# Kernel optimization log

Hardware: AMD Instinct MI355X
Metric: run time of the kernel (lower is better)

The kernel has to match this reference:

```python
import jax, jax.numpy as jnp
import numpy as np
from jax import lax

B, C, H, W = 16, 128, 64, 64
S = 16  # d_state


def setup_inputs() -> dict:
    key = jax.random.key(0)
    ks = jax.random.split(key, 12)
    d = {
        'x': jax.random.normal(ks[0], (B, C, H, W), jnp.float32),
        'conv_w': jax.random.normal(ks[1], (C, C, 3, 3), jnp.float32) * (1.0 / np.sqrt(C * 9)),
        'conv_b': jax.random.normal(ks[2], (C,), jnp.float32) * 0.01,
        'dt_w': jax.random.normal(ks[3], (C, C), jnp.float32) * (1.0 / np.sqrt(C)),
        'dt_b': jax.random.normal(ks[4], (C,), jnp.float32) * 0.01,
        'A': jax.random.normal(ks[5], (C, S), jnp.float32),
        'D': jax.random.normal(ks[6], (C,), jnp.float32),
        'g1_w': jax.random.normal(ks[7], (C, C), jnp.float32) * (1.0 / np.sqrt(C)),
        'g1_b': jax.random.normal(ks[8], (C,), jnp.float32) * 0.01,
        'g2_w': jax.random.normal(ks[9], (C, C), jnp.float32) * (1.0 / np.sqrt(C)),
        'g2_b': jax.random.normal(ks[10], (C,), jnp.float32) * 0.01,
    }
    return d


def _forward(x, conv_w, conv_b, dt_w, dt_b, A, D, g1_w, g1_b, g2_w, g2_b):
    identity = x
    # 3x3 conv, padding=1 (SAME)
    x = lax.conv_general_dilated(x, conv_w, (1, 1), 'SAME',
                                 dimension_numbers=('NCHW', 'OIHW', 'NCHW'))
    x = x + conv_b[None, :, None, None]
    # spectral gate: global avg pool -> 1x1 conv -> relu -> 1x1 conv -> sigmoid
    pooled = jnp.mean(x, axis=(2, 3))                       # [B, C]
    g = jax.nn.relu(jnp.einsum('bc,oc->bo', pooled, g1_w) + g1_b)
    g = jax.nn.sigmoid(jnp.einsum('bc,oc->bo', g, g2_w) + g2_b)
    x = x * g[:, :, None, None]
    # ssm scan over H*W tokens
    x_seq = x.transpose(0, 2, 3, 1).reshape(x.shape[0], H * W, C)  # [B, L, C]
    dt = jax.nn.sigmoid(jnp.einsum('blc,oc->blo', x_seq, dt_w) + dt_b)
    An = -jnp.exp(A)   # [C, S]
    Dp = jnp.exp(D)    # [C]

    def step(h, inp):
        xt, dtt = inp  # each [B, C]
        h = h * jnp.exp(An[None] * dtt[:, :, None]) + xt[:, :, None]  # [B, C, S]
        y = jnp.sum(h * An[None], axis=-1) + Dp * xt                   # [B, C]
        return h, y

    h0 = jnp.zeros((x.shape[0], C, S), x.dtype)
    xs = (x_seq.transpose(1, 0, 2), dt.transpose(1, 0, 2))  # [L, B, C]
    _, ys = lax.scan(step, h0, xs)                           # ys: [L, B, C]
    y = ys.transpose(1, 0, 2).reshape(x.shape[0], H, W, C).transpose(0, 3, 1, 2)
    return y + identity


def reference(x, conv_w, conv_b, dt_w, dt_b, A, D, g1_w, g1_b, g2_w, g2_b):
    return _forward(x, conv_w, conv_b, dt_w, dt_b, A, D, g1_w, g1_b, g2_w, g2_b)
```

## Files before the change

### kernel.cpp

```cpp
#include <hip/hip_runtime.h>
#include <hip/hip_bf16.h>
#include <stdint.h>

#define BB 16
#define CC 128
#define HH 64
#define WW 64
#define LL 4096
#define SS 16
#define NCH 64
#define CT 64

typedef __attribute__((ext_vector_type(2))) float f32x2;
typedef __attribute__((ext_vector_type(4))) float f32x4;
typedef __attribute__((ext_vector_type(8))) short short8;
typedef __attribute__((ext_vector_type(4))) unsigned int u32x4;

#define AS1 __attribute__((address_space(1)))
#define AS3 __attribute__((address_space(3)))

__device__ __forceinline__ float bf2f(unsigned short u) {
    union { unsigned int i; float f; } v;
    v.i = ((unsigned int)u) << 16;
    return v.f;
}
__device__ __forceinline__ float asf(unsigned int u) {
    union { unsigned int i; float f; } v;
    v.i = u;
    return v.f;
}
__device__ __forceinline__ unsigned short f2bf(float f) {
    union { float f; unsigned int i; } v;
    v.f = f;
    unsigned int x = v.i;
    return (unsigned short)((x + 0x7fffu + ((x >> 16) & 1u)) >> 16);
}
__device__ __forceinline__ float fexp2(float x) { return __builtin_amdgcn_exp2f(x); }

__global__ __launch_bounds__(256) void k0(const float* __restrict__ x, unsigned short* __restrict__ xT,
                                          const float* __restrict__ conv_w, const float* __restrict__ dt_w,
                                          const float* __restrict__ A, const float* __restrict__ Dv,
                                          const float* __restrict__ g1w, const float* __restrict__ g2w,
                                          short* __restrict__ wf, short* __restrict__ wdtf,
                                          float* __restrict__ An, float* __restrict__ An2, float* __restrict__ Dp,
                                          float* __restrict__ pooled, float* __restrict__ g1wT, float* __restrict__ g2wT) {
    __shared__ float lt[64][65];
    int bid = blockIdx.x;
    int tid = threadIdx.x;
    if (bid < 2048) {
        int b = bid >> 7, rem = bid & 127;
        int tt = rem >> 1, ct = rem & 1;
        int t0 = tt * 64, c0 = ct * 64;
        int colr = tid & 63, rowb = tid >> 6;
#pragma unroll
        for (int r = 0; r < 16; ++r) {
            int row = rowb + r * 4;
            lt[row][colr] = x[(size_t)(b * CC + c0 + row) * LL + t0 + colr];
        }
        __syncthreads();
#pragma unroll
        for (int r = 0; r < 16; ++r) {
            int trow = rowb + r * 4;
            xT[((size_t)b * LL + t0 + trow) * CC + c0 + colr] = f2bf(lt[colr][trow]);
        }
        return;
    }
    int idx = (bid - 2048) * 256 + tid;
    if (idx < 18432) {
        int lane = idx & 63, fr = idx >> 6;
        int nfg = fr & 7, ks = (fr >> 3) & 3, tp = fr >> 5;
        int dy = tp / 3, dx = tp % 3;
        int cout = nfg * 16 + (lane & 15);
        int cin0 = ks * 32 + (lane >> 4) * 8;
        short8 v;
#pragma unroll
        for (int j = 0; j < 8; ++j)
            v[j] = (short)f2bf(conv_w[((cout * CC + cin0 + j) * 3 + dy) * 3 + dx]);
        *(short8*)(wf + (size_t)idx * 8) = v;
    } else if (idx < 20480) {
        int i2 = idx - 18432;
        int lane = i2 & 63, fr = i2 >> 6;
        int nfg = fr & 7, ks = fr >> 3;
        int o = nfg * 16 + (lane & 15);
        int c0 = ks * 32 + (lane >> 4) * 8;
        short8 v;
#pragma unroll
        for (int j = 0; j < 8; ++j) v[j] = (short)f2bf(dt_w[o * CC + c0 + j]);
        *(short8*)(wdtf + (size_t)i2 * 8) = v;
    } else if (idx < 22528) {
        int i3 = idx - 20480;
        float a = -expf(A[i3]);
        An[i3] = a;
        An2[i3] = a * 1.4426950408889634f;
    } else if (idx < 22656) {
        int c = idx - 22528;
        Dp[c] = expf(Dv[c]);
    } else if (idx < 24704) {
        pooled[idx - 22656] = 0.f;
    } else if (idx < 41088) {
        int i = idx - 24704;
        int c = i >> 7, o = i & 127;
        g1wT[i] = g1w[o * 128 + c];
    } else if (idx < 57472) {
        int i = idx - 41088;
        int c = i >> 7, o = i & 127;
        g2wT[i] = g2w[o * 128 + c];
    }
}

__global__ __launch_bounds__(256) void k1(const unsigned short* __restrict__ xT,
                                          const short* __restrict__ wf,
                                          const float* __restrict__ conv_b,
                                          unsigned short* __restrict__ convT,
                                          float* __restrict__ pooled) {
    __shared__ __align__(16) unsigned short slab[3 * 66 * 128];
    int bid = blockIdx.x;
    int b = bid >> 6, h = bid & 63;
    int tid = threadIdx.x;
    int wave = tid >> 6, lane = tid & 63;

    if (tid < 96) {
        int dy = tid >> 5, r = (tid >> 4) & 1, j = tid & 15;
        u32x4 z = {0, 0, 0, 0};
        *(u32x4*)((char*)slab + dy * 16896 + (r ? 16640 : 0) + j * 16) = z;
    }
#pragma unroll
    for (int dy = 0; dy < 3; ++dy) {
        int hs = h + dy - 1;
        char* slabdy = (char*)slab + dy * 16896;
        if (hs >= 0 && hs < HH) {
            const char* src = (const char*)xT + (size_t)(b * LL + hs * 64) * 256;
#pragma unroll
            for (int i = 0; i < 4; ++i) {
                unsigned int Xbase = 256u + (unsigned)i * 4096u + (unsigned)wave * 1024u;
                unsigned int X = Xbase + (unsigned)lane * 16u;
                unsigned int tok = X >> 8;
                unsigned int srcoff = ((X & ~255u) - 256u) | ((X & 255u) ^ ((tok & 7u) << 4));
                __builtin_amdgcn_global_load_lds((const AS1 unsigned int*)(src + srcoff),
                                                 (AS3 unsigned int*)(slabdy + Xbase), 16, 0, 0);
            }
        } else {
            u32x4 z = {0, 0, 0, 0};
#pragma unroll
            for (int i = 0; i < 4; ++i)
                *(u32x4*)(slabdy + 256 + tid * 64 + i * 16) = z;
        }
    }
    __syncthreads();

    int lm = lane & 15, lg = lane >> 4;
    f32x4 acc[4][2];
#pragma unroll
    for (int m = 0; m < 4; ++m)
#pragma unroll
        for (int n = 0; n < 2; ++n) acc[m][n] = (f32x4){0.f, 0.f, 0.f, 0.f};

#pragma unroll
    for (int tp = 0; tp < 9; ++tp) {
        int dy = tp / 3, dx = tp % 3;
        const char* slabdy = (const char*)slab + dy * 16896;
#pragma unroll
        for (int ks = 0; ks < 4; ++ks) {
            short8 bf0 = *(const short8*)(wf + ((size_t)(((tp * 4 + ks) * 8) + wave * 2 + 0) * 64 + lane) * 8);
            short8 bf1 = *(const short8*)(wf + ((size_t)(((tp * 4 + ks) * 8) + wave * 2 + 1) * 64 + lane) * 8);
#pragma unroll
            for (int mf = 0; mf < 4; ++mf) {
                int tok = mf * 16 + lm + dx;
                unsigned int off = (unsigned)((tok * 256 + ks * 64 + lg * 16) ^ ((tok & 7) << 4));
                short8 af = *(const short8*)(slabdy + off);
                acc[mf][0] = __builtin_amdgcn_mfma_f32_16x16x32_bf16(af, bf0, acc[mf][0], 0, 0, 0);
                acc[mf][1] = __builtin_amdgcn_mfma_f32_16x16x32_bf16(af, bf1, acc[mf][1], 0, 0, 0);
            }
        }
    }

    int n0w = wave * 32;
    size_t tokbase = (size_t)(b * LL + h * 64);
    float psum[2] = {0.f, 0.f};
#pragma unroll
    for (int nf = 0; nf < 2; ++nf) {
        int n = n0w + nf * 16 + lm;
        float bias = conv_b[n];
#pragma unroll
        for (int mf = 0; mf < 4; ++mf)
#pragma unroll
            for (int r = 0; r < 4; ++r) {
                int w = mf * 16 + lg * 4 + r;
                float v = acc[mf][nf][r] + bias;
                convT[(tokbase + w) * CC + n] = f2bf(v);
                psum[nf] += v;
            }
    }
#pragma unroll
    for (int nf = 0; nf < 2; ++nf) {
        float s = psum[nf];
        s += __shfl_xor(s, 16);
        s += __shfl_xor(s, 32);
        if (lane < 16) atomicAdd(&pooled[b * CC + n0w + nf * 16 + lane], s);
    }
}

__global__ __launch_bounds__(256) void k3(const unsigned short* __restrict__ convT,
                                          const short* __restrict__ wdtf,
                                          const float* __restrict__ pooled,
                                          const float* __restrict__ g1wT, const float* __restrict__ g1b,
                                          const float* __restrict__ g2wT, const float* __restrict__ g2b,
                                          float* __restrict__ gate,
                                          const float* __restrict__ dt_b,
                                          const float* __restrict__ An2,
                                          unsigned short* __restrict__ dtT,
                                          unsigned int* __restrict__ xdt,
                                          float* __restrict__ hend, float* __restrict__ decay,
                                          int packed) {
    __shared__ __align__(16) unsigned short albuf[128 * 128];
    __shared__ __align__(16) unsigned short dtl[128 * 136];
    __shared__ float gl[128];
    float* meanr = (float*)dtl;
    float* garr  = ((float*)dtl) + 128;
    int bid = blockIdx.x;
    int b = bid >> 5, tile = bid & 31, t0 = tile * 128;
    int tid = threadIdx.x;
    int wave = tid >> 6, lane = tid & 63;

    if (tid < 128) meanr[tid] = pooled[b * CC + tid] * (1.f / 4096.f);
    __syncthreads();
    if (tid < 128) {
        float acc = g1b[tid];
        for (int c = 0; c < 128; ++c) acc += meanr[c] * g1wT[c * 128 + tid];
        garr[tid] = fmaxf(acc, 0.f);
    }
    __syncthreads();
    if (tid < 128) {
        float acc2 = g2b[tid];
        for (int c = 0; c < 128; ++c) acc2 += garr[c] * g2wT[c * 128 + tid];
        float gv = __builtin_amdgcn_rcpf(1.f + fexp2(-1.4426950408889634f * acc2));
        gl[tid] = gv;
        if (tile == 0) gate[b * CC + tid] = gv;
    }
    __syncthreads();

    const char* srcb = (const char*)convT + (size_t)(b * LL + t0) * 256;
#pragma unroll
    for (int i = 0; i < 8; ++i) {
        unsigned int byteoff = (unsigned)((i * 256 + tid) * 16);
        unsigned int tok = byteoff >> 8;
        unsigned int inner = byteoff & 255u;
        int c8 = (int)(inner >> 1);
        short8 v = *(const short8*)(srcb + (size_t)tok * 256 + inner);
#pragma unroll
        for (int j = 0; j < 8; ++j) {
            float f = bf2f((unsigned short)v[j]) * gl[c8 + j];
            v[j] = (short)f2bf(f);
        }
        *(short8*)((char*)albuf + (byteoff ^ ((tok & 7u) << 4))) = v;
    }
    __syncthreads();

    int lm = lane & 15, lg = lane >> 4;
    f32x4 acc[8][2];
#pragma unroll
    for (int m = 0; m < 8; ++m)
#pragma unroll
        for (int n = 0; n < 2; ++n) acc[m][n] = (f32x4){0.f, 0.f, 0.f, 0.f};
#pragma unroll
    for (int ks = 0; ks < 4; ++ks) {
        short8 bf0 = *(const short8*)(wdtf + ((size_t)((ks * 8) + wave * 2 + 0) * 64 + lane) * 8);
        short8 bf1 = *(const short8*)(wdtf + ((size_t)((ks * 8) + wave * 2 + 1) * 64 + lane) * 8);
#pragma unroll
        for (int mf = 0; mf < 8; ++mf) {
            int tok = mf * 16 + lm;
            unsigned int off = (unsigned)((tok * 256 + ks * 64 + lg * 16) ^ ((tok & 7) << 4));
            short8 af = *(const short8*)((const char*)albuf + off);
            acc[mf][0] = __builtin_amdgcn_mfma_f32_16x16x32_bf16(af, bf0, acc[mf][0], 0, 0, 0);
            acc[mf][1] = __builtin_amdgcn_mfma_f32_16x16x32_bf16(af, bf1, acc[mf][1], 0, 0, 0);
        }
    }
    __syncthreads();
#pragma unroll
    for (int nf = 0; nf < 2; ++nf) {
        int o = wave * 32 + nf * 16 + lm;
        float zb = dt_b[o];
#pragma unroll
        for (int mf = 0; mf < 8; ++mf)
#pragma unroll
            for (int r = 0; r < 4; ++r) {
                int tok = mf * 16 + lg * 4 + r;
                float z = acc[mf][nf][r] + zb;
                float d = __builtin_amdgcn_rcpf(1.f + fexp2(-1.4426950408889634f * z));
                unsigned short ub = f2bf(d);
                if (!packed) dtT[(size_t)(b * LL + t0 + tok) * CC + o] = ub;
                dtl[tok * 136 + o] = ub;
            }
    }
    __syncthreads();

    int half = tid >> 7, c = tid & 127;
    int ch = tile * 2 + half;
    float a2[SS], h[SS];
#pragma unroll
    for (int s = 0; s < SS; ++s) {
        a2[s] = An2[c * SS + s];
        h[s] = 0.f;
    }
    float sdt = 0.f;
    unsigned int* xdrow = xdt + ((size_t)b * CC + c) * LL + t0 + half * 64;
    for (int t4 = 0; t4 < 16; ++t4) {
        u32x4 pk;
#pragma unroll
        for (int j = 0; j < 4; ++j) {
            int t = t4 * 4 + j;
            int tokb = half * 64 + t;
            unsigned int xoff = ((unsigned)(tokb * 256 + c * 2)) ^ (((unsigned)tokb & 7u) << 4);
            unsigned short xu = *(const unsigned short*)((const char*)albuf + xoff);
            unsigned short du = dtl[tokb * 136 + c];
            float x = bf2f(xu);
            float d = bf2f(du);
            sdt += d;
#pragma unroll
            for (int s = 0; s < SS; ++s) h[s] = h[s] * fexp2(a2[s] * d) + x;
            pk[j] = (((unsigned int)du) << 16) | (unsigned int)xu;
        }
        if (packed) *(u32x4*)(xdrow + t4 * 4) = pk;
    }
    size_t base = ((size_t)(b * NCH + ch) * CC + c) * SS;
#pragma unroll
    for (int q = 0; q < 4; ++q) {
        f32x4 hv, dv;
#pragma unroll
        for (int j = 0; j < 4; ++j) {
            hv[j] = h[q * 4 + j];
            dv[j] = fexp2(a2[q * 4 + j] * sdt);
        }
        *(f32x4*)(hend + base + q * 4) = hv;
        *(f32x4*)(decay + base + q * 4) = dv;
    }
}

__global__ __launch_bounds__(256) void k5(const float* __restrict__ hend, const float* __restrict__ decay,
                                          float* __restrict__ H0) {
    int idx = blockIdx.x * 256 + threadIdx.x;
    int b = idx >> 11, rem = idx & 2047;
    float Hv = 0.f;
    for (int k = 0; k < NCH; ++k) {
        size_t base = (size_t)(b * NCH + k) * 2048 + rem;
        H0[base] = Hv;
        Hv = hend[base] + Hv * decay[base];
    }
}

__global__ __launch_bounds__(256, 4) void k6p(const unsigned int* __restrict__ xdt,
                                              const float* __restrict__ Antab,
                                              const float* __restrict__ An2tab,
                                              const float* __restrict__ Dp,
                                              const float* __restrict__ H0,
                                              const float* __restrict__ xin,
                                              float* __restrict__ out) {
    __shared__ unsigned short ylds[128][66];
    int bid = blockIdx.x;
    int b = bid >> 6, ch = bid & 63;
    int tid = threadIdx.x;
    int wave = tid >> 6, lane = tid & 63;
    int t0 = ch * CT;
    int c = wave * 32 + (lane & 31);
    int shalf = lane >> 5;
    int s0 = shalf * 8;

    f32x2 a22[4], anv[4], h2[4];
#pragma unroll
    for (int q = 0; q < 2; ++q) {
        f32x4 av = *(const f32x4*)(An2tab + c * SS + s0 + q * 4);
        f32x4 nv = *(const f32x4*)(Antab + c * SS + s0 + q * 4);
        a22[q * 2 + 0] = (f32x2){av[0], av[1]};
        a22[q * 2 + 1] = (f32x2){av[2], av[3]};
        anv[q * 2 + 0] = (f32x2){nv[0], nv[1]};
        anv[q * 2 + 1] = (f32x2){nv[2], nv[3]};
    }
    size_t hbase = ((size_t)(b * NCH + ch) * CC + c) * SS + s0;
#pragma unroll
    for (int q = 0; q < 2; ++q) {
        f32x4 hv = *(const f32x4*)(H0 + hbase + q * 4);
        h2[q * 2 + 0] = (f32x2){hv[0], hv[1]};
        h2[q * 2 + 1] = (f32x2){hv[2], hv[3]};
    }
    float dpc = (shalf == 0) ? Dp[c] : 0.f;
    const u32x4* xdp = (const u32x4*)(xdt + ((size_t)b * CC + c) * LL + t0);

#pragma unroll 4
    for (int t4 = 0; t4 < 16; ++t4) {
        u32x4 w4 = xdp[t4];
#pragma unroll
        for (int j = 0; j < 4; ++j) {
            unsigned int w = w4[j];
            float x = asf(w << 16);
            float d = asf(w & 0xffff0000u);
            f32x2 x2 = {x, x};
            f32x2 d2 = {d, d};
            f32x2 y2 = {0.f, 0.f};
#pragma unroll
            for (int q = 0; q < 4; ++q) {
                f32x2 tq = a22[q] * d2;
                f32x2 e2;
                e2.x = fexp2(tq.x);
                e2.y = fexp2(tq.y);
                h2[q] = h2[q] * e2 + x2;
                y2 += h2[q] * anv[q];
            }
            float yp = y2.x + y2.y + dpc * x;
            float yo = yp + __shfl_xor(yp, 32);
            if (shalf == 0) ylds[c][t4 * 4 + j] = f2bf(yo);
        }
    }
    __syncthreads();

    int tt = tid & 63, wq = tid >> 6;
    size_t outbase = (size_t)b * CC * LL + t0 + tt;
#pragma unroll 4
    for (int rr = 0; rr < 32; ++rr) {
        int row = rr * 4 + wq;
        size_t gi = outbase + (size_t)row * LL;
        out[gi] = bf2f(ylds[row][tt]) + xin[gi];
    }
}

__global__ __launch_bounds__(256, 4) void k6f(const unsigned short* __restrict__ convT,
                                              const unsigned short* __restrict__ dtT,
                                              const float* __restrict__ gate,
                                              const float* __restrict__ Antab,
                                              const float* __restrict__ An2tab,
                                              const float* __restrict__ Dp,
                                              const float* __restrict__ H0,
                                              const float* __restrict__ xin,
                                              float* __restrict__ out) {
    __shared__ unsigned short ylds[128][66];
    int bid = blockIdx.x;
    int b = bid >> 6, ch = bid & 63;
    int tid = threadIdx.x;
    int wave = tid >> 6, lane = tid & 63;
    int t0 = ch * CT;
    int c = wave * 32 + (lane & 31);
    int shalf = lane >> 5;
    int s0 = shalf * 8;

    float a2[8], an[8], h[8];
#pragma unroll
    for (int q = 0; q < 2; ++q) {
        f32x4 av = *(const f32x4*)(An2tab + c * SS + s0 + q * 4);
        f32x4 nv = *(const f32x4*)(Antab + c * SS + s0 + q * 4);
#pragma unroll
        for (int j = 0; j < 4; ++j) { a2[q * 4 + j] = av[j]; an[q * 4 + j] = nv[j]; }
    }
    size_t hbase = ((size_t)(b * NCH + ch) * CC + c) * SS + s0;
#pragma unroll
    for (int q = 0; q < 2; ++q) {
        f32x4 hv = *(const f32x4*)(H0 + hbase + q * 4);
#pragma unroll
        for (int j = 0; j < 4; ++j) h[q * 4 + j] = hv[j];
    }
    float g = gate[b * CC + c];
    float dpc = (shalf == 0) ? Dp[c] : 0.f;
    const unsigned short* xp = convT + (size_t)(b * LL + t0) * CC + c;
    const unsigned short* dp = dtT + (size_t)(b * LL + t0) * CC + c;

#pragma unroll 4
    for (int t = 0; t < CT; ++t) {
        float x = bf2f(xp[t * CC]) * g;
        float d = bf2f(dp[t * CC]);
        float y0 = dpc * x, y1 = 0.f;
#pragma unroll
        for (int s = 0; s < 8; ++s) {
            h[s] = h[s] * fexp2(a2[s] * d) + x;
            if (s & 1) y1 += h[s] * an[s]; else y0 += h[s] * an[s];
        }
        float yp = y0 + y1;
        float yo = yp + __shfl_xor(yp, 32);
        if (shalf == 0) ylds[c][t] = f2bf(yo);
    }
    __syncthreads();

    int tt = tid & 63, wq = tid >> 6;
    size_t outbase = (size_t)b * CC * LL + t0 + tt;
#pragma unroll 4
    for (int rr = 0; rr < 32; ++rr) {
        int row = rr * 4 + wq;
        size_t gi = outbase + (size_t)row * LL;
        out[gi] = bf2f(ylds[row][tt]) + xin[gi];
    }
}

extern "C" void kernel_launch(void* const* d_in, const int* in_sizes, int n_in,
                              void* d_out, int out_size, void* d_ws, size_t ws_size,
                              hipStream_t stream) {
    const float* x      = (const float*)d_in[0];
    const float* conv_w = (const float*)d_in[1];
    const float* conv_b = (const float*)d_in[2];
    const float* dt_w   = (const float*)d_in[3];
    const float* dt_b   = (const float*)d_in[4];
    const float* A      = (const float*)d_in[5];
    const float* D      = (const float*)d_in[6];
    const float* g1w    = (const float*)d_in[7];
    const float* g1b    = (const float*)d_in[8];
    const float* g2w    = (const float*)d_in[9];
    const float* g2b    = (const float*)d_in[10];
    float* outp         = (float*)d_out;
    char* ws = (char*)d_ws;

    const bool P = (ws_size >= 67600896ull);

    unsigned short* xT;
    float *hend, *decay, *H0, *g1wT, *g2wT, *pooled, *gate, *Antab, *An2tab, *Dp;
    unsigned short *convT, *dtT;
    unsigned int* xdt;
    short *wf, *wdtf;

    if (P) {
        xT     = (unsigned short*)(ws + 0);
        hend   = (float*)(ws + 0);
        decay  = (float*)(ws + 8388608);
        convT  = (unsigned short*)(ws + 16777216);
        H0     = (float*)(ws + 16777216);
        xdt    = (unsigned int*)(ws + 33554432);
        dtT    = (unsigned short*)(ws + 33554432);
        wf     = (short*)(ws + 67108864);
        wdtf   = (short*)(ws + 67403776);
        pooled = (float*)(ws + 67436544);
        gate   = (float*)(ws + 67444736);
        Antab  = (float*)(ws + 67452928);
        An2tab = (float*)(ws + 67461120);
        Dp     = (float*)(ws + 67469312);
        g1wT   = (float*)(ws + 67469824);
        g2wT   = (float*)(ws + 67535360);
    } else {
        xT     = (unsigned short*)(ws + 0);
        hend   = (float*)(ws + 0);
        decay  = (float*)(ws + 8388608);
        convT  = (unsigned short*)(ws + 16777216);
        dtT    = (unsigned short*)(ws + 33554432);
        xdt    = (unsigned int*)(ws + 33554432);
        H0     = (float*)(ws + 50331648);
        g1wT   = (float*)(ws + 50331648);
        g2wT   = (float*)(ws + 50397184);
        wf     = (short*)(ws + 58720256);
        wdtf   = (short*)(ws + 59015168);
        pooled = (float*)(ws + 59047936);
        gate   = (float*)(ws + 59056128);
        Antab  = (float*)(ws + 59064320);
        An2tab = (float*)(ws + 59072512);
        Dp     = (float*)(ws + 59080704);
    }

    hipLaunchKernelGGL(k0, dim3(2273), dim3(256), 0, stream, x, xT, conv_w, dt_w, A, D, g1w, g2w,
                       wf, wdtf, Antab, An2tab, Dp, pooled, g1wT, g2wT);
    hipLaunchKernelGGL(k1, dim3(1024), dim3(256), 0, stream, xT, wf, conv_b, convT, pooled);
    hipLaunchKernelGGL(k3, dim3(512), dim3(256), 0, stream, convT, wdtf, pooled, g1wT, g1b, g2wT, g2b,
                       gate, dt_b, An2tab, dtT, xdt, hend, decay, (int)P);
    hipLaunchKernelGGL(k5, dim3(128), dim3(256), 0, stream, hend, decay, H0);
    if (P) {
        hipLaunchKernelGGL(k6p, dim3(1024), dim3(256), 0, stream, (const unsigned int*)xdt,
                           Antab, An2tab, Dp, H0, x, outp);
    } else {
        hipLaunchKernelGGL(k6f, dim3(1024), dim3(256), 0, stream, convT, dtT, gate,
                           Antab, An2tab, Dp, H0, x, outp);
    }
}
```

Measured before the change: 120.9 us.

## Store packed x/dt buffer token-major for coalesced writes and reads

Result: slower. 127.1 us (median of 2 runs) (+5.1%).

```diff
diff --git a/kernel.cpp b/kernel.cpp
--- a/kernel.cpp
+++ b/kernel.cpp
@@ -294,6 +294,23 @@
     }
     __syncthreads();
 
+    if (packed) {
+        unsigned int* xdblk = xdt + ((size_t)b * LL + t0) * CC;
+        int tq = tid >> 5, c0 = (tid & 31) * 4;
+#pragma unroll
+        for (int k = 0; k < 16; ++k) {
+            int t = k * 8 + tq;
+            unsigned int xoff = ((unsigned)(t * 256 + c0 * 2)) ^ (((unsigned)t & 7u) << 4);
+            const unsigned short* xu4 = (const unsigned short*)((const char*)albuf + xoff);
+            const unsigned short* du4 = &dtl[t * 136 + c0];
+            u32x4 w4;
+#pragma unroll
+            for (int j = 0; j < 4; ++j)
+                w4[j] = (((unsigned int)du4[j]) << 16) | (unsigned int)xu4[j];
+            *(u32x4*)(xdblk + (size_t)t * CC + c0) = w4;
+        }
+    }
+
     int half = tid >> 7, c = tid & 127;
     int ch = tile * 2 + half;
     float a2[SS], h[SS];
@@ -303,24 +320,15 @@
         h[s] = 0.f;
     }
     float sdt = 0.f;
-    unsigned int* xdrow = xdt + ((size_t)b * CC + c) * LL + t0 + half * 64;
-    for (int t4 = 0; t4 < 16; ++t4) {
-        u32x4 pk;
-#pragma unroll
-        for (int j = 0; j < 4; ++j) {
-            int t = t4 * 4 + j;
-            int tokb = half * 64 + t;
-            unsigned int xoff = ((unsigned)(tokb * 256 + c * 2)) ^ (((unsigned)tokb & 7u) << 4);
-            unsigned short xu = *(const unsigned short*)((const char*)albuf + xoff);
-            unsigned short du = dtl[tokb * 136 + c];
-            float x = bf2f(xu);
-            float d = bf2f(du);
-            sdt += d;
-#pragma unroll
-            for (int s = 0; s < SS; ++s) h[s] = h[s] * fexp2(a2[s] * d) + x;
-            pk[j] = (((unsigned int)du) << 16) | (unsigned int)xu;
-        }
-        if (packed) *(u32x4*)(xdrow + t4 * 4) = pk;
+#pragma unroll 4
+    for (int t = 0; t < CT; ++t) {
+        int tokb = half * 64 + t;
+        unsigned int xoff = ((unsigned)(tokb * 256 + c * 2)) ^ (((unsigned)tokb & 7u) << 4);
+        float x = bf2f(*(const unsigned short*)((const char*)albuf + xoff));
+        float d = bf2f(dtl[tokb * 136 + c]);
+        sdt += d;
+#pragma unroll
+        for (int s = 0; s < SS; ++s) h[s] = h[s] * fexp2(a2[s] * d) + x;
     }
     size_t base = ((size_t)(b * NCH + ch) * CC + c) * SS;
 #pragma unroll
@@ -383,32 +391,28 @@
         h2[q * 2 + 1] = (f32x2){hv[2], hv[3]};
     }
     float dpc = (shalf == 0) ? Dp[c] : 0.f;
-    const u32x4* xdp = (const u32x4*)(xdt + ((size_t)b * CC + c) * LL + t0);
-
-#pragma unroll 4
-    for (int t4 = 0; t4 < 16; ++t4) {
-        u32x4 w4 = xdp[t4];
-#pragma unroll
-        for (int j = 0; j < 4; ++j) {
-            unsigned int w = w4[j];
-            float x = asf(w << 16);
-            float d = asf(w & 0xffff0000u);
-            f32x2 x2 = {x, x};
-            f32x2 d2 = {d, d};
-            f32x2 y2 = {0.f, 0.f};
-#pragma unroll
-            for (int q = 0; q < 4; ++q) {
-                f32x2 tq = a22[q] * d2;
-                f32x2 e2;
-                e2.x = fexp2(tq.x);
-                e2.y = fexp2(tq.y);
-                h2[q] = h2[q] * e2 + x2;
-                y2 += h2[q] * anv[q];
-            }
-            float yp = y2.x + y2.y + dpc * x;
-            float yo = yp + __shfl_xor(yp, 32);
-            if (shalf == 0) ylds[c][t4 * 4 + j] = f2bf(yo);
-        }
+    const unsigned int* xdp = xdt + ((size_t)b * LL + t0) * CC + c;
+
+#pragma unroll 8
+    for (int t = 0; t < CT; ++t) {
+        unsigned int w = xdp[(size_t)t * CC];
+        float x = asf(w << 16);
+        float d = asf(w & 0xffff0000u);
+        f32x2 x2 = {x, x};
+        f32x2 d2 = {d, d};
+        f32x2 y2 = {0.f, 0.f};
+#pragma unroll
+        for (int q = 0; q < 4; ++q) {
+            f32x2 tq = a22[q] * d2;
+            f32x2 e2;
+            e2.x = fexp2(tq.x);
+            e2.y = fexp2(tq.y);
+            h2[q] = h2[q] * e2 + x2;
+            y2 += h2[q] * anv[q];
+        }
+        float yp = y2.x + y2.y + dpc * x;
+        float yo = yp + __shfl_xor(yp, 32);
+        if (shalf == 0) ylds[c][t] = f2bf(yo);
     }
     __syncthreads();
 
```
